# Optimization experiments

Measured on AMD Instinct MI355X. Metric: run time of the kernel, lower is better.

## Reference

```python
import jax, jax.numpy as jnp
import numpy as np

DIM = 384
HEADS = 8


def setup_inputs() -> dict:
    key = jax.random.key(0)
    ks = jax.random.split(key, 6)
    B, H, W = 8, 64, 64
    N, C = H * W, DIM
    s = 0.02  # init scale for weights
    return {
        "x": jax.random.normal(ks[0], (B, N, C), jnp.float32),
        # depthwise conv: OIHW with feature_group_count=C -> [C,1,3,3]
        "w_sr": jax.random.normal(ks[1], (C, 1, 3, 3), jnp.float32) * s,
        "b_sr": jax.random.normal(ks[2], (C,), jnp.float32) * s,
        "ln_g": jnp.ones((C,), jnp.float32),
        "ln_b": jnp.zeros((C,), jnp.float32),
        # linears stored [in, out] (torch stores [out,in]; random so equivalent)
        "w_qkv": jax.random.normal(ks[3], (C, 3 * C), jnp.float32) * s,
        "w_proj": jax.random.normal(ks[4], (C, C), jnp.float32) * s,
        "b_proj": jax.random.normal(ks[5], (C,), jnp.float32) * s,
        "H": 64,
        "W": 64,
    }


def reference(x, w_sr, b_sr, ln_g, ln_b, w_qkv, w_proj, b_proj, H, W):
    B, N, C = x.shape
    h = HEADS
    d = C // h
    shortcut = x

    # --- depthwise conv branch: sr(x) -> LN -> GELU -> residual add ---
    x_img = x.transpose(0, 2, 1).reshape(B, C, H, W)
    x_sr = jax.lax.conv_general_dilated(
        x_img, w_sr, window_strides=(1, 1), padding="SAME",
        dimension_numbers=("NCHW", "OIHW", "NCHW"), feature_group_count=C,
    ) + b_sr[None, :, None, None]
    x_sr = x_sr.reshape(B, C, N).transpose(0, 2, 1)  # [B, N, C]
    mu = x_sr.mean(-1, keepdims=True)
    var = x_sr.var(-1, keepdims=True)
    xn = (x_sr - mu) * jax.lax.rsqrt(var + 1e-5) * ln_g + ln_b
    x = x + jax.nn.gelu(xn, approximate=False)  # torch GELU is erf-based

    # --- linear attention ---
    qkv = (x @ w_qkv).reshape(B, N, 3, h, d)
    q = qkv[:, :, 0].transpose(0, 2, 1, 3)  # [B, h, N, d]
    k = qkv[:, :, 1].transpose(0, 2, 1, 3)
    v = qkv[:, :, 2].transpose(0, 2, 1, 3)
    q = jax.nn.softmax(q, axis=-2)  # softmax over sequence dim N
    k = jax.nn.softmax(k, axis=-1)  # softmax over head_dim
    ctx = jnp.einsum("bhnd,bhne->bhde", k, v)          # [B, h, d, d]
    attn = jnp.einsum("bhnd,bhde->bhne", q, ctx)       # [B, h, N, d]
    attn = attn.transpose(0, 2, 1, 3).reshape(B, N, C)

    out = attn @ w_proj + b_proj
    return out + shortcut
```

## Files before the change

### kernel.cpp

```cpp
#include <hip/hip_runtime.h>

typedef unsigned short u16;
typedef u16   u16x8  __attribute__((ext_vector_type(8)));
typedef short short8 __attribute__((ext_vector_type(8)));
typedef float floatx4 __attribute__((ext_vector_type(4)));
typedef float f4     __attribute__((ext_vector_type(4)));

#define BB 8
#define NN 4096
#define CC 384

__device__ __forceinline__ u16 f2bf(float f){
  unsigned u = __float_as_uint(f);
  u += 0x7FFFu + ((u >> 16) & 1u);
  return (u16)(u >> 16);
}
__device__ __forceinline__ float bf2f(u16 u){ return __uint_as_float(((unsigned)u) << 16); }

__global__ __launch_bounds__(256) void k_prep(const float* __restrict__ wqkv, u16* __restrict__ WT)
{
  const int cg = blockIdx.x % 18;
  const int kg = blockIdx.x / 18;
  const int c0 = cg << 6, k0 = kg << 6;
  const int tid = threadIdx.x;
  __shared__ u16 t[64][72];
#pragma unroll
  for (int i = 0; i < 4; i++) {
    int idx = tid + (i << 8);
    int r = idx >> 4, c4 = (idx & 15) << 2;
    f4 v = *(const f4*)(wqkv + (size_t)(k0 + r) * 1152 + c0 + c4);
#pragma unroll
    for (int j = 0; j < 4; j++) t[c4 + j][r] = f2bf(v[j]);
  }
  __syncthreads();
#pragma unroll
  for (int i = 0; i < 2; i++) {
    int idx = tid + (i << 8);
    int c = idx >> 3, j = (idx & 7) << 3;
    *(u16x8*)(WT + (size_t)(c0 + c) * 384 + k0 + j) = *(const u16x8*)&t[c][j];
  }
}

__global__ __launch_bounds__(384) void k_conv_ln_gelu(
    const float* __restrict__ x, const float* __restrict__ w_sr, const float* __restrict__ b_sr,
    const float* __restrict__ ln_g, const float* __restrict__ ln_b, u16* __restrict__ xa16)
{
  const int blk = blockIdx.x;
  const int b = blk >> 9;
  const int hh = (blk >> 3) & 63;
  const int ww0 = (blk & 7) << 3;
  const int c = threadIdx.x;

  float wgt[9];
#pragma unroll
  for (int i = 0; i < 9; i++) wgt[i] = w_sr[c * 9 + i];
  const float lg = ln_g[c], lb = ln_b[c];
  const float bias = b_sr[c];

  float rowv[3][10];
#pragma unroll
  for (int r = 0; r < 3; r++) {
    int y = hh + r - 1;
    bool yok = (unsigned)y < 64u;
#pragma unroll
    for (int j = 0; j < 10; j++) {
      int xx = ww0 + j - 1;
      bool ok = yok && ((unsigned)xx < 64u);
      rowv[r][j] = ok ? x[((size_t)((b << 12) + (y << 6) + xx)) * CC + c] : 0.f;
    }
  }

  float acc[8];
#pragma unroll
  for (int p = 0; p < 8; p++) {
    float a = bias;
#pragma unroll
    for (int r = 0; r < 3; r++)
#pragma unroll
      for (int j = 0; j < 3; j++)
        a += rowv[r][p + j] * wgt[r * 3 + j];
    acc[p] = a;
  }

  __shared__ float ls1[6][8], ls2[6][8], mb[2][8];
  const int wid = threadIdx.x >> 6, lane = threadIdx.x & 63;
#pragma unroll
  for (int p = 0; p < 8; p++) {
    float s1 = acc[p], s2 = acc[p] * acc[p];
#pragma unroll
    for (int o = 32; o > 0; o >>= 1) { s1 += __shfl_down(s1, o); s2 += __shfl_down(s2, o); }
    if (lane == 0) { ls1[wid][p] = s1; ls2[wid][p] = s2; }
  }
  __syncthreads();
  if (threadIdx.x < 8) {
    int p = threadIdx.x;
    float a = 0.f, q = 0.f;
#pragma unroll
    for (int i = 0; i < 6; i++) { a += ls1[i][p]; q += ls2[i][p]; }
    float mean = a * (1.0f / CC);
    float var  = q * (1.0f / CC) - mean * mean;
    mb[0][p] = mean; mb[1][p] = rsqrtf(var + 1e-5f);
  }
  __syncthreads();
#pragma unroll
  for (int p = 0; p < 8; p++) {
    float xn = (acc[p] - mb[0][p]) * mb[1][p] * lg + lb;
    float g  = 0.5f * xn * (1.0f + erff(xn * 0.70710678118654752f));
    size_t pix = (size_t)(b << 12) + (hh << 6) + ww0 + p;
    xa16[pix * CC + c] = f2bf(rowv[1][p + 1] + g);
  }
}

__global__ __launch_bounds__(256) void k_kvctx(
    const u16* __restrict__ xa16, const u16* __restrict__ WT, float* __restrict__ ctx)
{
  const int rt = blockIdx.x, h = blockIdx.y;
  const int n0 = rt << 8;
  const int bh = ((rt >> 4) << 3) + h;
  const int tid = threadIdx.x;
  const int wv = tid >> 6, lane = tid & 63, l15 = lane & 15, quad = lane >> 4;

  __shared__ __attribute__((aligned(16))) char smem[50688];
  u16 (*lA)[72]   = (u16(*)[72])smem;
  u16 (*lW)[72]   = (u16(*)[72])(smem + 36864);
  u16 (*lkT)[264] = (u16(*)[264])smem;
  u16 (*lvT)[264] = (u16(*)[264])(smem + 25344);
  float (*pctx)[2304] = (float(*)[2304])smem;

  floatx4 acc[24];
  const floatx4 z = {0.f, 0.f, 0.f, 0.f};
#pragma unroll
  for (int i = 0; i < 24; i++) acc[i] = z;

  for (int k0 = 0; k0 < 384; k0 += 64) {
    __syncthreads();
#pragma unroll
    for (int i = 0; i < 8; i++) {
      int idx = tid + (i << 8);
      int r = idx >> 3, c8 = (idx & 7) << 3;
      *(u16x8*)&lA[r][c8] = *(const u16x8*)(xa16 + (size_t)(n0 + r) * 384 + k0 + c8);
    }
#pragma unroll
    for (int i = 0; i < 3; i++) {
      int idx = tid + (i << 8);
      int c = idx >> 3, j = (idx & 7) << 3;
      int gcol = (c < 48) ? (384 + h * 48 + c) : (720 + h * 48 + c);
      *(u16x8*)&lW[c][j] = *(const u16x8*)(WT + (size_t)gcol * 384 + k0 + j);
    }
    __syncthreads();
#pragma unroll
    for (int rt4 = 0; rt4 < 4; rt4++) {
      int m = (wv << 6) + (rt4 << 4) + l15;
#pragma unroll
      for (int kk = 0; kk < 2; kk++) {
        short8 af = *(const short8*)&lA[m][(kk << 5) + (quad << 3)];
#pragma unroll
        for (int ct = 0; ct < 6; ct++) {
          short8 bf = *(const short8*)&lW[(ct << 4) + l15][(kk << 5) + (quad << 3)];
          acc[rt4 * 6 + ct] = __builtin_amdgcn_mfma_f32_16x16x32_bf16(af, bf, acc[rt4 * 6 + ct], 0, 0, 0);
        }
      }
    }
  }

#pragma unroll
  for (int rt4 = 0; rt4 < 4; rt4++) {
#pragma unroll
    for (int rr = 0; rr < 4; rr++) {
      float x0 = acc[rt4 * 6 + 0][rr];
      float x1 = acc[rt4 * 6 + 1][rr];
      float x2 = acc[rt4 * 6 + 2][rr];
      float m = fmaxf(fmaxf(x0, x1), x2);
#pragma unroll
      for (int o = 8; o >= 1; o >>= 1) m = fmaxf(m, __shfl_xor(m, o));
      float e0 = expf(x0 - m), e1 = expf(x1 - m), e2 = expf(x2 - m);
      float s = e0 + e1 + e2;
#pragma unroll
      for (int o = 8; o >= 1; o >>= 1) s += __shfl_xor(s, o);
      float inv = 1.0f / s;
      acc[rt4 * 6 + 0][rr] = e0 * inv;
      acc[rt4 * 6 + 1][rr] = e1 * inv;
      acc[rt4 * 6 + 2][rr] = e2 * inv;
    }
  }

  __syncthreads();

#pragma unroll
  for (int rt4 = 0; rt4 < 4; rt4++) {
    int rowb = (wv << 6) + (rt4 << 4) + (quad << 2);
#pragma unroll
    for (int ct = 0; ct < 6; ct++) {
      int col = (ct << 4) + l15;
      u16 (*dst)[264] = (ct < 3) ? lkT : lvT;
      int c = (ct < 3) ? col : (col - 48);
#pragma unroll
      for (int rp = 0; rp < 2; rp++) {
        unsigned lo = f2bf(acc[rt4 * 6 + ct][(rp << 1) + 0]);
        unsigned hi = f2bf(acc[rt4 * 6 + ct][(rp << 1) + 1]);
        *(unsigned*)&dst[c][rowb + (rp << 1)] = lo | (hi << 16);
      }
    }
  }
  __syncthreads();

  floatx4 c2[9];
#pragma unroll
  for (int i = 0; i < 9; i++) c2[i] = z;
#pragma unroll
  for (int kk2 = 0; kk2 < 2; kk2++) {
    int rb = (wv << 6) + (kk2 << 5) + (quad << 3);
    short8 ak[3], av[3];
#pragma unroll
    for (int t = 0; t < 3; t++) {
      ak[t] = *(const short8*)&lkT[(t << 4) + l15][rb];
      av[t] = *(const short8*)&lvT[(t << 4) + l15][rb];
    }
#pragma unroll
    for (int dt = 0; dt < 3; dt++)
#pragma unroll
      for (int et = 0; et < 3; et++)
        c2[dt * 3 + et] = __builtin_amdgcn_mfma_f32_16x16x32_bf16(ak[dt], av[et], c2[dt * 3 + et], 0, 0, 0);
  }
  __syncthreads();

#pragma unroll
  for (int dt = 0; dt < 3; dt++)
#pragma unroll
    for (int et = 0; et < 3; et++)
#pragma unroll
      for (int rr = 0; rr < 4; rr++) {
        int d = (dt << 4) + (quad << 2) + rr;
        int e = (et << 4) + l15;
        pctx[wv][d * 48 + e] = c2[dt * 3 + et][rr];
      }
  __syncthreads();
#pragma unroll
  for (int i = 0; i < 9; i++) {
    int cell = tid + (i << 8);
    float s = pctx[0][cell] + pctx[1][cell] + pctx[2][cell] + pctx[3][cell];
    atomicAdd(&ctx[(size_t)bh * 2304 + cell], s);
  }
}

__global__ __launch_bounds__(256) void k_qsumk(
    const u16* __restrict__ xa16, const u16* __restrict__ WT, float* __restrict__ S,
    u16* __restrict__ P16)
{
  const int bm = blockIdx.x;
  const int b = bm >> 6;
  const int tid = threadIdx.x;
  const int wv = tid >> 6, lane = tid & 63, l15 = lane & 15, quad = lane >> 4;
  __shared__ __attribute__((aligned(16))) u16 lA[64][72];
  __shared__ __attribute__((aligned(16))) u16 lB[64][72];

  floatx4 acc[24];
  const floatx4 z = {0.f, 0.f, 0.f, 0.f};
#pragma unroll
  for (int i = 0; i < 24; i++) acc[i] = z;

  for (int k0 = 0; k0 < 384; k0 += 64) {
    __syncthreads();
#pragma unroll
    for (int i = 0; i < 2; i++) {
      int idx = tid + (i << 8);
      int r = idx >> 3, c8 = (idx & 7) << 3;
      *(u16x8*)&lA[r][c8] = *(const u16x8*)(xa16 + (size_t)((bm << 6) + r) * 384 + k0 + c8);
    }
    for (int ctg = 0; ctg < 6; ctg++) {
      __syncthreads();
#pragma unroll
      for (int i = 0; i < 2; i++) {
        int idx = tid + (i << 8);
        int c = idx >> 3, j = (idx & 7) << 3;
        *(u16x8*)&lB[c][j] = *(const u16x8*)(WT + (size_t)((ctg << 6) + c) * 384 + k0 + j);
      }
      __syncthreads();
      int m = (wv << 4) + l15;
#pragma unroll
      for (int kk = 0; kk < 2; kk++) {
        short8 af = *(const short8*)&lA[m][(kk << 5) + (quad << 3)];
#pragma unroll
        for (int c4i = 0; c4i < 4; c4i++) {
          short8 bf = *(const short8*)&lB[(c4i << 4) + l15][(kk << 5) + (quad << 3)];
          acc[(ctg << 2) + c4i] = __builtin_amdgcn_mfma_f32_16x16x32_bf16(af, bf, acc[(ctg << 2) + c4i], 0, 0, 0);
        }
      }
    }
  }
#pragma unroll
  for (int t = 0; t < 24; t++) {
    int col = (t << 4) + l15;
    float e0 = expf(acc[t][0]), e1 = expf(acc[t][1]), e2 = expf(acc[t][2]), e3 = expf(acc[t][3]);
    int rowb = (bm << 6) + (wv << 4) + (quad << 2);
    P16[(size_t)(rowb + 0) * 384 + col] = f2bf(e0);
    P16[(size_t)(rowb + 1) * 384 + col] = f2bf(e1);
    P16[(size_t)(rowb + 2) * 384 + col] = f2bf(e2);
    P16[(size_t)(rowb + 3) * 384 + col] = f2bf(e3);
    float s = e0 + e1 + e2 + e3;
    s += __shfl_down(s, 32);
    s += __shfl_down(s, 16);
    if (lane < 16) atomicAdd(&S[b * 384 + (t << 4) + lane], s);
  }
}

__global__ __launch_bounds__(256) void k_w2(
    const float* __restrict__ ctx, const float* __restrict__ S,
    const float* __restrict__ wp, u16* __restrict__ W2T)
{
  const int bh = blockIdx.x;
  const int b = bh >> 3, h = bh & 7;
  const int c0 = blockIdx.y << 7;
  const int tid = threadIdx.x;
  __shared__ float rs[48];
  __shared__ float c2[48][48];
  __shared__ float lwp[48][128];
  __shared__ u16 tr[128][48];
  if (tid < 48) rs[tid] = 1.0f / S[b * 384 + h * 48 + tid];
  __syncthreads();
#pragma unroll
  for (int i = 0; i < 9; i++) {
    int cell = tid + (i << 8);
    int d = cell / 48, e = cell - d * 48;
    c2[d][e] = ctx[(size_t)bh * 2304 + cell] * rs[d];
  }
#pragma unroll
  for (int i = 0; i < 24; i++) {
    int idx = tid + (i << 8);
    int e = idx >> 7, c = idx & 127;
    lwp[e][c] = wp[(size_t)(h * 48 + e) * 384 + c0 + c];
  }
  __syncthreads();
  const int c = tid & 127;
  const int dbase = tid >> 7;
#pragma unroll
  for (int it = 0; it < 24; it++) {
    int d = (it << 1) + dbase;
    float s = 0.f;
#pragma unroll
    for (int e = 0; e < 48; e++) s += c2[d][e] * lwp[e][c];
    tr[c][d] = f2bf(s);
  }
  __syncthreads();
  const int cc = tid >> 1, half = tid & 1;
#pragma unroll
  for (int i = 0; i < 3; i++) {
    u16x8 v = *(const u16x8*)&tr[cc][half * 24 + (i << 3)];
    *(u16x8*)(W2T + ((size_t)b * 384 + c0 + cc) * 384 + h * 48 + half * 24 + (i << 3)) = v;
  }
}

__global__ __launch_bounds__(256) void k_qproj(
    const u16* __restrict__ P16, const u16* __restrict__ W2T,
    const float* __restrict__ bias, const float* __restrict__ x, float* __restrict__ out)
{
  const int bm = blockIdx.x;
  const int b = bm >> 6;
  const int tid = threadIdx.x;
  const int wv = tid >> 6, lane = tid & 63, l15 = lane & 15, quad = lane >> 4;
  __shared__ __attribute__((aligned(16))) u16 lB[64][72];
  __shared__ __attribute__((aligned(16))) u16 P[64][392];

  floatx4 acc[24];
  const floatx4 z = {0.f, 0.f, 0.f, 0.f};
#pragma unroll
  for (int i = 0; i < 24; i++) acc[i] = z;

#pragma unroll
  for (int i = 0; i < 12; i++) {
    int idx = tid + (i << 8);
    int r = idx / 48, ch = idx - r * 48, j = ch << 3;
    *(u16x8*)&P[r][j] = *(const u16x8*)(P16 + (size_t)((bm << 6) + r) * 384 + j);
  }

  for (int k0 = 0; k0 < 384; k0 += 64) {
    for (int ctg = 0; ctg < 6; ctg++) {
      __syncthreads();
#pragma unroll
      for (int i = 0; i < 2; i++) {
        int idx = tid + (i << 8);
        int c = idx >> 3, j = (idx & 7) << 3;
        *(u16x8*)&lB[c][j] = *(const u16x8*)(W2T + ((size_t)b * 384 + (ctg << 6) + c) * 384 + k0 + j);
      }
      __syncthreads();
      int m = (wv << 4) + l15;
#pragma unroll
      for (int kk = 0; kk < 2; kk++) {
        short8 af = *(const short8*)&P[m][k0 + (kk << 5) + (quad << 3)];
#pragma unroll
        for (int c4i = 0; c4i < 4; c4i++) {
          short8 bf = *(const short8*)&lB[(c4i << 4) + l15][(kk << 5) + (quad << 3)];
          acc[(ctg << 2) + c4i] = __builtin_amdgcn_mfma_f32_16x16x32_bf16(af, bf, acc[(ctg << 2) + c4i], 0, 0, 0);
        }
      }
    }
  }
#pragma unroll
  for (int t = 0; t < 24; t++) {
    int col = (t << 4) + l15;
#pragma unroll
    for (int rr = 0; rr < 4; rr++) {
      int row = (bm << 6) + (wv << 4) + (quad << 2) + rr;
      float v = acc[t][rr] + bias[col] + x[(size_t)row * 384 + col];
      out[(size_t)row * 384 + col] = v;
    }
  }
}

extern "C" void kernel_launch(void* const* d_in, const int* in_sizes, int n_in,
                              void* d_out, int out_size, void* d_ws, size_t ws_size,
                              hipStream_t stream)
{
  const float* x      = (const float*)d_in[0];
  const float* w_sr   = (const float*)d_in[1];
  const float* b_sr   = (const float*)d_in[2];
  const float* ln_g   = (const float*)d_in[3];
  const float* ln_b   = (const float*)d_in[4];
  const float* w_qkv  = (const float*)d_in[5];
  const float* w_proj = (const float*)d_in[6];
  const float* b_proj = (const float*)d_in[7];
  float* out = (float*)d_out;

  float* S   = (float*)d_ws;
  float* ctx = (float*)((char*)d_ws + 12288);
  u16*   WT  = (u16*)((char*)d_ws + 602112);
  u16*   W2T = (u16*)((char*)d_ws + 1486848);
  u16*   xa16= (u16*)((char*)d_ws + 3846144);
  u16*   P16 = xa16;

  hipMemsetAsync(d_ws, 0, 602112, stream);

  k_prep<<<108, 256, 0, stream>>>(w_qkv, WT);
  k_conv_ln_gelu<<<BB * 512, 384, 0, stream>>>(x, w_sr, b_sr, ln_g, ln_b, xa16);
  k_kvctx<<<dim3(128, 8), 256, 0, stream>>>(xa16, WT, ctx);
  k_qsumk<<<512, 256, 0, stream>>>(xa16, WT, S, P16);
  k_w2<<<dim3(64, 3), 256, 0, stream>>>(ctx, S, w_proj, W2T);
  k_qproj<<<512, 256, 0, stream>>>(P16, W2T, b_proj, x, out);
}
```

Before: 297.8 us.

## Load GEMM A/B fragments directly from global, shrink kvctx tile and restage B

k_kvctx now processes 128-row tiles, twice as many blocks, and reads both A and W fragments straight from global memory into registers, dropping the LDS staging and barriers of the K-loop. k_qsumk and k_qproj now stage the whole 384-column B slab per 32-wide K step in LDS, with one barrier pair per step instead of per 64-column group. Their A fragments are read directly from global, and the full P row copy into LDS is removed. The aim is fewer synchronisations, less LDS traffic and more parallelism in kvctx. The cost is uncoalesced direct global fragment loads and more atomics on ctx.

```diff
diff --git a/kernel.cpp b/kernel.cpp
--- a/kernel.cpp
+++ b/kernel.cpp
@@ -115,56 +115,45 @@
     const u16* __restrict__ xa16, const u16* __restrict__ WT, float* __restrict__ ctx)
 {
   const int rt = blockIdx.x, h = blockIdx.y;
-  const int n0 = rt << 8;
-  const int bh = ((rt >> 4) << 3) + h;
+  const int n0 = rt << 7;
+  const int bh = ((rt >> 5) << 3) + h;
   const int tid = threadIdx.x;
   const int wv = tid >> 6, lane = tid & 63, l15 = lane & 15, quad = lane >> 4;
 
-  __shared__ __attribute__((aligned(16))) char smem[50688];
-  u16 (*lA)[72]   = (u16(*)[72])smem;
-  u16 (*lW)[72]   = (u16(*)[72])(smem + 36864);
-  u16 (*lkT)[264] = (u16(*)[264])smem;
-  u16 (*lvT)[264] = (u16(*)[264])(smem + 25344);
+  __shared__ __attribute__((aligned(16))) char smem[36864];
+  u16 (*lkT)[136] = (u16(*)[136])smem;
+  u16 (*lvT)[136] = (u16(*)[136])(smem + 13056);
   float (*pctx)[2304] = (float(*)[2304])smem;
 
-  floatx4 acc[24];
+  floatx4 acc[12];
   const floatx4 z = {0.f, 0.f, 0.f, 0.f};
 #pragma unroll
-  for (int i = 0; i < 24; i++) acc[i] = z;
+  for (int i = 0; i < 12; i++) acc[i] = z;
 
   for (int k0 = 0; k0 < 384; k0 += 64) {
-    __syncthreads();
-#pragma unroll
-    for (int i = 0; i < 8; i++) {
-      int idx = tid + (i << 8);
-      int r = idx >> 3, c8 = (idx & 7) << 3;
-      *(u16x8*)&lA[r][c8] = *(const u16x8*)(xa16 + (size_t)(n0 + r) * 384 + k0 + c8);
-    }
-#pragma unroll
-    for (int i = 0; i < 3; i++) {
-      int idx = tid + (i << 8);
-      int c = idx >> 3, j = (idx & 7) << 3;
+    short8 af[2][2];
+#pragma unroll
+    for (int rt4 = 0; rt4 < 2; rt4++)
+#pragma unroll
+      for (int kk = 0; kk < 2; kk++)
+        af[rt4][kk] = *(const short8*)(xa16 +
+            (size_t)(n0 + (wv << 5) + (rt4 << 4) + l15) * 384 + k0 + (kk << 5) + (quad << 3));
+#pragma unroll
+    for (int ct = 0; ct < 6; ct++) {
+      int c = (ct << 4) + l15;
       int gcol = (c < 48) ? (384 + h * 48 + c) : (720 + h * 48 + c);
-      *(u16x8*)&lW[c][j] = *(const u16x8*)(WT + (size_t)gcol * 384 + k0 + j);
-    }
-    __syncthreads();
-#pragma unroll
-    for (int rt4 = 0; rt4 < 4; rt4++) {
-      int m = (wv << 6) + (rt4 << 4) + l15;
 #pragma unroll
       for (int kk = 0; kk < 2; kk++) {
-        short8 af = *(const short8*)&lA[m][(kk << 5) + (quad << 3)];
-#pragma unroll
-        for (int ct = 0; ct < 6; ct++) {
-          short8 bf = *(const short8*)&lW[(ct << 4) + l15][(kk << 5) + (quad << 3)];
-          acc[rt4 * 6 + ct] = __builtin_amdgcn_mfma_f32_16x16x32_bf16(af, bf, acc[rt4 * 6 + ct], 0, 0, 0);
-        }
+        short8 bf = *(const short8*)(WT + (size_t)gcol * 384 + k0 + (kk << 5) + (quad << 3));
+#pragma unroll
+        for (int rt4 = 0; rt4 < 2; rt4++)
+          acc[rt4 * 6 + ct] = __builtin_amdgcn_mfma_f32_16x16x32_bf16(af[rt4][kk], bf, acc[rt4 * 6 + ct], 0, 0, 0);
       }
     }
   }
 
 #pragma unroll
-  for (int rt4 = 0; rt4 < 4; rt4++) {
+  for (int rt4 = 0; rt4 < 2; rt4++) {
 #pragma unroll
     for (int rr = 0; rr < 4; rr++) {
       float x0 = acc[rt4 * 6 + 0][rr];
@@ -184,15 +173,13 @@
     }
   }
 
-  __syncthreads();
-
-#pragma unroll
-  for (int rt4 = 0; rt4 < 4; rt4++) {
-    int rowb = (wv << 6) + (rt4 << 4) + (quad << 2);
+#pragma unroll
+  for (int rt4 = 0; rt4 < 2; rt4++) {
+    int rowb = (wv << 5) + (rt4 << 4) + (quad << 2);
 #pragma unroll
     for (int ct = 0; ct < 6; ct++) {
       int col = (ct << 4) + l15;
-      u16 (*dst)[264] = (ct < 3) ? lkT : lvT;
+      u16 (*dst)[136] = (ct < 3) ? lkT : lvT;
       int c = (ct < 3) ? col : (col - 48);
 #pragma unroll
       for (int rp = 0; rp < 2; rp++) {
@@ -207,9 +194,8 @@
   floatx4 c2[9];
 #pragma unroll
   for (int i = 0; i < 9; i++) c2[i] = z;
-#pragma unroll
-  for (int kk2 = 0; kk2 < 2; kk2++) {
-    int rb = (wv << 6) + (kk2 << 5) + (quad << 3);
+  {
+    int rb = (wv << 5) + (quad << 3);
     short8 ak[3], av[3];
 #pragma unroll
     for (int t = 0; t < 3; t++) {
@@ -251,41 +237,29 @@
   const int b = bm >> 6;
   const int tid = threadIdx.x;
   const int wv = tid >> 6, lane = tid & 63, l15 = lane & 15, quad = lane >> 4;
-  __shared__ __attribute__((aligned(16))) u16 lA[64][72];
-  __shared__ __attribute__((aligned(16))) u16 lB[64][72];
+  __shared__ __attribute__((aligned(16))) u16 lB[384][40];
 
   floatx4 acc[24];
   const floatx4 z = {0.f, 0.f, 0.f, 0.f};
 #pragma unroll
   for (int i = 0; i < 24; i++) acc[i] = z;
 
-  for (int k0 = 0; k0 < 384; k0 += 64) {
+  const size_t arow = (size_t)((bm << 6) + (wv << 4) + l15) * 384;
+
+  for (int k0 = 0; k0 < 384; k0 += 32) {
     __syncthreads();
 #pragma unroll
-    for (int i = 0; i < 2; i++) {
+    for (int i = 0; i < 6; i++) {
       int idx = tid + (i << 8);
-      int r = idx >> 3, c8 = (idx & 7) << 3;
-      *(u16x8*)&lA[r][c8] = *(const u16x8*)(xa16 + (size_t)((bm << 6) + r) * 384 + k0 + c8);
-    }
-    for (int ctg = 0; ctg < 6; ctg++) {
-      __syncthreads();
-#pragma unroll
-      for (int i = 0; i < 2; i++) {
-        int idx = tid + (i << 8);
-        int c = idx >> 3, j = (idx & 7) << 3;
-        *(u16x8*)&lB[c][j] = *(const u16x8*)(WT + (size_t)((ctg << 6) + c) * 384 + k0 + j);
-      }
-      __syncthreads();
-      int m = (wv << 4) + l15;
-#pragma unroll
-      for (int kk = 0; kk < 2; kk++) {
-        short8 af = *(const short8*)&lA[m][(kk << 5) + (quad << 3)];
-#pragma unroll
-        for (int c4i = 0; c4i < 4; c4i++) {
-          short8 bf = *(const short8*)&lB[(c4i << 4) + l15][(kk << 5) + (quad << 3)];
-          acc[(ctg << 2) + c4i] = __builtin_amdgcn_mfma_f32_16x16x32_bf16(af, bf, acc[(ctg << 2) + c4i], 0, 0, 0);
-        }
-      }
+      int cl = idx >> 2, ko = (idx & 3) << 3;
+      *(u16x8*)&lB[cl][ko] = *(const u16x8*)(WT + (size_t)cl * 384 + k0 + ko);
+    }
+    __syncthreads();
+    short8 af = *(const short8*)(xa16 + arow + k0 + (quad << 3));
+#pragma unroll
+    for (int ct = 0; ct < 24; ct++) {
+      short8 bf = *(const short8*)&lB[(ct << 4) + l15][quad << 3];
+      acc[ct] = __builtin_amdgcn_mfma_f32_16x16x32_bf16(af, bf, acc[ct], 0, 0, 0);
     }
   }
 #pragma unroll
@@ -358,41 +332,29 @@
   const int b = bm >> 6;
   const int tid = threadIdx.x;
   const int wv = tid >> 6, lane = tid & 63, l15 = lane & 15, quad = lane >> 4;
-  __shared__ __attribute__((aligned(16))) u16 lB[64][72];
-  __shared__ __attribute__((aligned(16))) u16 P[64][392];
+  __shared__ __attribute__((aligned(16))) u16 lB[384][40];
 
   floatx4 acc[24];
   const floatx4 z = {0.f, 0.f, 0.f, 0.f};
 #pragma unroll
   for (int i = 0; i < 24; i++) acc[i] = z;
 
-#pragma unroll
-  for (int i = 0; i < 12; i++) {
-    int idx = tid + (i << 8);
-    int r = idx / 48, ch = idx - r * 48, j = ch << 3;
-    *(u16x8*)&P[r][j] = *(const u16x8*)(P16 + (size_t)((bm << 6) + r) * 384 + j);
-  }
-
-  for (int k0 = 0; k0 < 384; k0 += 64) {
-    for (int ctg = 0; ctg < 6; ctg++) {
-      __syncthreads();
-#pragma unroll
-      for (int i = 0; i < 2; i++) {
-        int idx = tid + (i << 8);
-        int c = idx >> 3, j = (idx & 7) << 3;
-        *(u16x8*)&lB[c][j] = *(const u16x8*)(W2T + ((size_t)b * 384 + (ctg << 6) + c) * 384 + k0 + j);
-      }
-      __syncthreads();
-      int m = (wv << 4) + l15;
-#pragma unroll
-      for (int kk = 0; kk < 2; kk++) {
-        short8 af = *(const short8*)&P[m][k0 + (kk << 5) + (quad << 3)];
-#pragma unroll
-        for (int c4i = 0; c4i < 4; c4i++) {
-          short8 bf = *(const short8*)&lB[(c4i << 4) + l15][(kk << 5) + (quad << 3)];
-          acc[(ctg << 2) + c4i] = __builtin_amdgcn_mfma_f32_16x16x32_bf16(af, bf, acc[(ctg << 2) + c4i], 0, 0, 0);
-        }
-      }
+  const size_t arow = (size_t)((bm << 6) + (wv << 4) + l15) * 384;
+
+  for (int k0 = 0; k0 < 384; k0 += 32) {
+    __syncthreads();
+#pragma unroll
+    for (int i = 0; i < 6; i++) {
+      int idx = tid + (i << 8);
+      int cl = idx >> 2, ko = (idx & 3) << 3;
+      *(u16x8*)&lB[cl][ko] = *(const u16x8*)(W2T + ((size_t)b * 384 + cl) * 384 + k0 + ko);
+    }
+    __syncthreads();
+    short8 af = *(const short8*)(P16 + arow + k0 + (quad << 3));
+#pragma unroll
+    for (int ct = 0; ct < 24; ct++) {
+      short8 bf = *(const short8*)&lB[(ct << 4) + l15][quad << 3];
+      acc[ct] = __builtin_amdgcn_mfma_f32_16x16x32_bf16(af, bf, acc[ct], 0, 0, 0);
     }
   }
 #pragma unroll
@@ -432,7 +394,7 @@
 
   k_prep<<<108, 256, 0, stream>>>(w_qkv, WT);
   k_conv_ln_gelu<<<BB * 512, 384, 0, stream>>>(x, w_sr, b_sr, ln_g, ln_b, xa16);
-  k_kvctx<<<dim3(128, 8), 256, 0, stream>>>(xa16, WT, ctx);
+  k_kvctx<<<dim3(256, 8), 256, 0, stream>>>(xa16, WT, ctx);
   k_qsumk<<<512, 256, 0, stream>>>(xa16, WT, S, P16);
   k_w2<<<dim3(64, 3), 256, 0, stream>>>(ctx, S, w_proj, W2T);
   k_qproj<<<512, 256, 0, stream>>>(P16, W2T, b_proj, x, out);
```

New measurement: 342.9 us. +15.2%, slower.
